# Kernel optimization log

Measured on AMD Instinct MI355X. Metric: run time of the kernel, lower is better.

Reference implementation:

```python
import jax, jax.numpy as jnp
import numpy as np

NUM_EMBEDDINGS = 512
EMBEDDING_DIM = 64
COMMITMENT_COST = 0.25


def setup_inputs() -> dict:
    key = jax.random.key(0)
    k1, k2 = jax.random.split(key)
    inputs = jax.random.normal(k1, (32, EMBEDDING_DIM, 64, 64), dtype=jnp.float32)
    # nn.Embedding weight init: uniform(-1/K, 1/K)
    weight = jax.random.uniform(
        k2, (NUM_EMBEDDINGS, EMBEDDING_DIM), dtype=jnp.float32,
        minval=-1.0 / NUM_EMBEDDINGS, maxval=1.0 / NUM_EMBEDDINGS)
    return {"inputs": inputs, "weight": weight}


def reference(inputs, weight):
    # NCHW -> NHWC
    x = jnp.transpose(inputs, (0, 2, 3, 1))
    B, H, W, D = x.shape
    flat = x.reshape(-1, D)  # [N, D]
    # squared L2 distances to each code: [N, K]
    distances = (jnp.sum(flat * flat, axis=1, keepdims=True)
                 - 2.0 * flat @ weight.T
                 + jnp.sum(weight * weight, axis=1))
    idx = jnp.argmin(distances, axis=1)  # [N]
    # one-hot @ weight == gather (one-hot entries are exactly 0/1)
    quantized = jnp.take(weight, idx, axis=0).reshape(B, H, W, D)
    e_latent_loss = jnp.mean((jax.lax.stop_gradient(quantized) - x) ** 2)
    q_latent_loss = jnp.mean((quantized - jax.lax.stop_gradient(x)) ** 2)
    loss = q_latent_loss + COMMITMENT_COST * e_latent_loss
    # straight-through estimator
    quantized_st = x + jax.lax.stop_gradient(quantized - x)
    discrete_latent = idx.reshape(B, H, W)
    quantized_out = jnp.transpose(quantized_st, (0, 3, 1, 2))  # NHWC -> NCHW
    return discrete_latent, quantized_out, loss
```

## Files before the change

kernel.cpp:

```cpp
#include <hip/hip_runtime.h>

typedef unsigned long long ull;

#define NUM_K   512
#define DIM     64
#define N_ROWS  (32 * 64 * 64)
#define HW      4096
#define CHW     (64 * 4096)

#define IDX_OFF  0
#define Q_OFF    N_ROWS
#define LOSS_OFF (N_ROWS + 32 * 64 * 4096)

#define CAP     8
#define TILE_R  128
#define NBLK    (N_ROWS / TILE_R)

#define WK1S    1.0e-4f
#define WK2S    2.0e-5f

#define WS_W2_OFF    32768
#define WS_W2H_OFF   33280
#define WS_SWMAX_OFF 33792
#define WS_LSL_BYTE  147456
#define WS_NEED      (147456 + NBLK * 8)

typedef __attribute__((ext_vector_type(8)))  short bf16x8;
typedef __attribute__((ext_vector_type(16))) float f32x16;

typedef unsigned uGLB __attribute__((address_space(1)));
typedef unsigned uLDS __attribute__((address_space(3)));
#define GLD16(g, l) __builtin_amdgcn_global_load_lds((const uGLB*)(g), (uLDS*)(l), 16, 0, 0)

#define NP_SUMSQ64(SRC, DST)                                                   \
    do {                                                                       \
        float r_[8];                                                           \
        _Pragma("unroll")                                                      \
        for (int j_ = 0; j_ < 8; ++j_) r_[j_] = __fmul_rn((SRC)[j_], (SRC)[j_]); \
        _Pragma("unroll")                                                      \
        for (int i_ = 8; i_ < 64; i_ += 8) {                                   \
            _Pragma("unroll")                                                  \
            for (int j_ = 0; j_ < 8; ++j_)                                     \
                r_[j_] = __fadd_rn(r_[j_], __fmul_rn((SRC)[i_ + j_], (SRC)[i_ + j_])); \
        }                                                                      \
        (DST) = __fadd_rn(__fadd_rn(__fadd_rn(r_[0], r_[1]), __fadd_rn(r_[2], r_[3])), \
                          __fadd_rn(__fadd_rn(r_[4], r_[5]), __fadd_rn(r_[6], r_[7]))); \
    } while (0)

#define NP_SUMSQ64_G(XC, DST)                                                  \
    do {                                                                       \
        float r_[8];                                                           \
        _Pragma("unroll")                                                      \
        for (int j_ = 0; j_ < 8; ++j_) {                                       \
            float v_ = (XC)[(size_t)j_ * HW];                                  \
            r_[j_] = __fmul_rn(v_, v_);                                        \
        }                                                                      \
        _Pragma("unroll")                                                      \
        for (int i_ = 8; i_ < 64; i_ += 8) {                                   \
            _Pragma("unroll")                                                  \
            for (int j_ = 0; j_ < 8; ++j_) {                                   \
                float v_ = (XC)[(size_t)(i_ + j_) * HW];                       \
                r_[j_] = __fadd_rn(r_[j_], __fmul_rn(v_, v_));                 \
            }                                                                  \
        }                                                                      \
        (DST) = __fadd_rn(__fadd_rn(__fadd_rn(r_[0], r_[1]), __fadd_rn(r_[2], r_[3])), \
                          __fadd_rn(__fadd_rn(r_[4], r_[5]), __fadd_rn(r_[6], r_[7]))); \
    } while (0)

__device__ __forceinline__ unsigned bf16rn(float f) {
    unsigned u = __float_as_uint(f);
    return (u + 0x7fffu + ((u >> 16) & 1u)) >> 16;
}
__device__ __forceinline__ float bf2f(unsigned h) { return __uint_as_float(h << 16); }
__device__ __forceinline__ unsigned pk2(float lo, float hi) {
    return bf16rn(lo) | (bf16rn(hi) << 16);
}

__device__ __forceinline__ float evald(const float* __restrict__ xr,
                                       const float* __restrict__ wc,
                                       float A, float w2c) {
    float m = 0.0f;
    #pragma unroll
    for (int d = 0; d < DIM; ++d) m = __fmaf_rn(xr[d], wc[d], m);
    return __fadd_rn(__fsub_rn(A, __fmul_rn(2.0f, m)), w2c);
}
__device__ __forceinline__ float evald_g(const float* __restrict__ xcol,
                                         const float* __restrict__ wc,
                                         float A, float w2c) {
    float m = 0.0f;
    #pragma unroll
    for (int d = 0; d < DIM; ++d) m = __fmaf_rn(xcol[(size_t)d * HW], wc[d], m);
    return __fadd_rn(__fsub_rn(A, __fmul_rn(2.0f, m)), w2c);
}

__global__ __launch_bounds__(64) void vq_prep8(const float* __restrict__ weight,
                                               unsigned* __restrict__ ws) {
    const int c = blockIdx.x * 64 + threadIdx.x;
    const int T = c >> 5, m = c & 31;
    const float* wr = weight + c * DIM;
    float wv[DIM];
    #pragma unroll
    for (int d = 0; d < DIM; d += 4) {
        float4 t4 = *(const float4*)&wr[d];
        wv[d] = t4.x; wv[d + 1] = t4.y; wv[d + 2] = t4.z; wv[d + 3] = t4.w;
    }
    float s; NP_SUMSQ64(wv, s);
    ((float*)(ws + WS_W2_OFF))[c]  = s;
    ((float*)(ws + WS_W2H_OFF))[c] = 0.5f * s;
    float sa = 0.0f;
    #pragma unroll
    for (int d = 0; d < DIM; ++d) sa = __fadd_rn(sa, fabsf(wv[d]));
    float sv = sa * 1.0002f + 1e-7f;

    #pragma unroll
    for (int s4 = 0; s4 < 4; ++s4) {
        const int gH = (T * 4 + s4) * 2, gL = gH + 1;
        #pragma unroll
        for (int kh = 0; kh < 2; ++kh) {
            unsigned hu[4], lu[4];
            #pragma unroll
            for (int p = 0; p < 4; ++p) {
                float e0 = wv[16 * s4 + 8 * kh + 2 * p];
                float e1 = wv[16 * s4 + 8 * kh + 2 * p + 1];
                unsigned h0 = bf16rn(e0), h1 = bf16rn(e1);
                float r0 = __fsub_rn(e0, bf2f(h0));
                float r1 = __fsub_rn(e1, bf2f(h1));
                hu[p] = h0 | (h1 << 16);
                lu[p] = bf16rn(r0) | (bf16rn(r1) << 16);
            }
            const int slot = (m + 32 * kh) * 4;
            *(uint4*)&ws[gH * 256 + slot] = make_uint4(hu[0], hu[1], hu[2], hu[3]);
            *(uint4*)&ws[gL * 256 + slot] = make_uint4(lu[0], lu[1], lu[2], lu[3]);
        }
    }
    #pragma unroll
    for (int mk = 1; mk <= 32; mk <<= 1) sv = fmaxf(sv, __shfl_xor(sv, mk));
    if (threadIdx.x == 0) ((float*)(ws + WS_SWMAX_OFF))[blockIdx.x] = sv;
}

__global__ __launch_bounds__(256, 3) void vq_mfma8(const float* __restrict__ x_in,
                                                   const float* __restrict__ weight,
                                                   const unsigned* __restrict__ frg,
                                                   const float* __restrict__ w2g,
                                                   const float* __restrict__ w2h,
                                                   double* __restrict__ lslots,
                                                   float* __restrict__ out) {
    __shared__ __align__(16) unsigned dbuf[2][4096];
    __shared__ int   cntL[TILE_R];
    __shared__ unsigned short listL[TILE_R * CAP];
    __shared__ int   ilds[TILE_R];
    __shared__ float wsum[4];

    const int tid   = threadIdx.x;
    const int lane  = tid & 63;
    const int wid   = tid >> 6;
    const int wbase = wid * 32;
    const int n31   = lane & 31;
    const int kh    = lane >> 5;

    const int rowbase = blockIdx.x * TILE_R;
    const int b       = rowbase >> 12;
    const int hw0     = rowbase & 4095;
    const float* xb   = x_in + (size_t)b * CHW + hw0;

    #pragma unroll
    for (int i = 0; i < 4; ++i) {
        int sg = wid * 4 + i;
        GLD16(frg + sg * 256 + lane * 4, &dbuf[0][sg * 256]);
    }

    bf16x8 bh[4], bl[4];
    float mx = 0.0f;
    const float* xp = xb + wbase + n31;
    #pragma unroll
    for (int s = 0; s < 4; ++s) {
        union { unsigned u[4]; bf16x8 v; } ch, cl;
        #pragma unroll
        for (int p = 0; p < 4; ++p) {
            const int k0 = 16 * s + 8 * kh + 2 * p;
            float x0 = xp[(size_t)k0 * HW];
            float x1 = xp[(size_t)(k0 + 1) * HW];
            mx = fmaxf(mx, fmaxf(fabsf(x0), fabsf(x1)));
            float e0 = -x0, e1 = -x1;
            unsigned h0 = bf16rn(e0), h1 = bf16rn(e1);
            float r0 = __fsub_rn(e0, bf2f(h0));
            float r1 = __fsub_rn(e1, bf2f(h1));
            ch.u[p] = h0 | (h1 << 16);
            cl.u[p] = bf16rn(r0) | (bf16rn(r1) << 16);
        }
        bh[s] = ch.v;
        bl[s] = cl.v;
    }
    mx = fmaxf(mx, __shfl_xor(mx, 32));
    if (tid < TILE_R) cntL[tid] = 0;

    const float* swp = (const float*)(frg + WS_SWMAX_OFF);
    float SWMAX = swp[0];
    #pragma unroll
    for (int i = 1; i < 8; ++i) SWMAX = fmaxf(SWMAX, swp[i]);
    const float gthr = __fmaf_rn(WK1S * mx, 2.0f * SWMAX, WK2S);
    float thr = 3.4e38f;
    __syncthreads();

    for (int c = 0; c < 8; ++c) {
        const int par = c & 1;
        if (c < 7) {
            const int nxt = par ^ 1;
            #pragma unroll
            for (int i = 0; i < 4; ++i) {
                int sg = wid * 4 + i;
                GLD16(frg + (c + 1) * 4096 + sg * 256 + lane * 4,
                      &dbuf[nxt][sg * 256]);
            }
        }

        f32x16 acc0, acc1;
        {
            const float* wa = w2h + (2 * c) * 32 + 4 * kh;
            float4 a0 = *(const float4*)&wa[0];
            float4 a1 = *(const float4*)&wa[8];
            float4 a2 = *(const float4*)&wa[16];
            float4 a3 = *(const float4*)&wa[24];
            acc0[0]=a0.x; acc0[1]=a0.y; acc0[2]=a0.z; acc0[3]=a0.w;
            acc0[4]=a1.x; acc0[5]=a1.y; acc0[6]=a1.z; acc0[7]=a1.w;
            acc0[8]=a2.x; acc0[9]=a2.y; acc0[10]=a2.z; acc0[11]=a2.w;
            acc0[12]=a3.x; acc0[13]=a3.y; acc0[14]=a3.z; acc0[15]=a3.w;
            const float* wb = w2h + (2 * c + 1) * 32 + 4 * kh;
            float4 c0 = *(const float4*)&wb[0];
            float4 c1 = *(const float4*)&wb[8];
            float4 c2 = *(const float4*)&wb[16];
            float4 c3 = *(const float4*)&wb[24];
            acc1[0]=c0.x; acc1[1]=c0.y; acc1[2]=c0.z; acc1[3]=c0.w;
            acc1[4]=c1.x; acc1[5]=c1.y; acc1[6]=c1.z; acc1[7]=c1.w;
            acc1[8]=c2.x; acc1[9]=c2.y; acc1[10]=c2.z; acc1[11]=c2.w;
            acc1[12]=c3.x; acc1[13]=c3.y; acc1[14]=c3.z; acc1[15]=c3.w;
        }

        #pragma unroll
        for (int s = 0; s < 4; ++s) {
            bf16x8 ah0 = *(const bf16x8*)&dbuf[par][(s * 2 + 0) * 256 + lane * 4];
            bf16x8 al0 = *(const bf16x8*)&dbuf[par][(s * 2 + 1) * 256 + lane * 4];
            bf16x8 ah1 = *(const bf16x8*)&dbuf[par][(8 * 256) + (s * 2 + 0) * 256 + lane * 4];
            bf16x8 al1 = *(const bf16x8*)&dbuf[par][(8 * 256) + (s * 2 + 1) * 256 + lane * 4];
            acc0 = __builtin_amdgcn_mfma_f32_32x32x16_bf16(ah0, bh[s], acc0, 0, 0, 0);
            acc1 = __builtin_amdgcn_mfma_f32_32x32x16_bf16(ah1, bh[s], acc1, 0, 0, 0);
            acc0 = __builtin_amdgcn_mfma_f32_32x32x16_bf16(al0, bh[s], acc0, 0, 0, 0);
            acc1 = __builtin_amdgcn_mfma_f32_32x32x16_bf16(al1, bh[s], acc1, 0, 0, 0);
            acc0 = __builtin_amdgcn_mfma_f32_32x32x16_bf16(ah0, bl[s], acc0, 0, 0, 0);
            acc1 = __builtin_amdgcn_mfma_f32_32x32x16_bf16(ah1, bl[s], acc1, 0, 0, 0);
        }

        #pragma unroll
        for (int tl = 0; tl < 2; ++tl) {
            float tmin = 3.4e38f;
            #pragma unroll
            for (int r = 0; r < 16; ++r)
                tmin = fminf(tmin, (tl ? acc1[r] : acc0[r]));
            float tlr = fminf(tmin, __shfl_xor(tmin, 32));
            thr = fminf(thr, __fadd_rn(tlr, gthr));
            if (tmin <= thr) {
                const int cb = (2 * c + tl) * 32 + 4 * kh;
                const int rr = wbase + n31;
                #pragma unroll
                for (int r = 0; r < 16; ++r) {
                    float tv = (tl ? acc1[r] : acc0[r]);
                    if (tv <= thr) {
                        int code = cb + (r & 3) + 8 * (r >> 2);
                        int cn = atomicAdd(&cntL[rr], 1);
                        if (cn < CAP) listL[rr * CAP + cn] = (unsigned short)code;
                    }
                }
            }
        }

        __syncthreads();
    }

    if (lane < 32) {
        const int r   = wbase + lane;
        const int cnt = cntL[r];
        if (cnt == 1) {
            int bi = listL[r * CAP];
            ilds[r] = bi;
            out[IDX_OFF + rowbase + r] = (float)bi;
        } else if (cnt >= 2 && cnt <= CAP) {
            const float* xcol = xb + r;
            float A; NP_SUMSQ64_G(xcol, A);
            float bd = 3.4e38f; int bi = 1 << 30;
            for (int t2 = 0; t2 < cnt; ++t2) {
                int cd = listL[r * CAP + t2];
                float d2 = evald_g(xcol, weight + cd * DIM, A, w2g[cd]);
                if (d2 < bd || (d2 == bd && cd < bi)) { bd = d2; bi = cd; }
            }
            ilds[r] = bi;
            out[IDX_OFF + rowbase + r] = (float)bi;
        }
    }
    for (int rr = 0; rr < 32; ++rr) {
        int r   = wbase + rr;
        int cnt = cntL[r];
        if (cnt < 1 || cnt > CAP) {
            const float* xcol = xb + r;
            float A; NP_SUMSQ64_G(xcol, A);
            float bd = 3.4e38f; int bi = 1 << 30;
            #pragma unroll
            for (int t2 = 0; t2 < 8; ++t2) {
                int cd = t2 * 64 + lane;
                float d2 = evald_g(xcol, weight + cd * DIM, A, w2g[cd]);
                if (d2 < bd || (d2 == bd && cd < bi)) { bd = d2; bi = cd; }
            }
            ull key = ((ull)__float_as_uint(bd) << 32) | (unsigned)bi;
            #pragma unroll
            for (int mk = 1; mk <= 32; mk <<= 1) {
                ull o = __shfl_xor(key, mk);
                if (o < key) key = o;
            }
            if (lane == 0) {
                int bi2 = (int)(key & 0xffffffffu);
                ilds[r] = bi2;
                out[IDX_OFF + rowbase + r] = (float)bi2;
            }
        }
    }
    __syncthreads();

    const int row = wbase + (lane & 31);
    const int dh  = (lane >> 5) << 5;
    const float* xcol = xb + row;
    const float* wr2  = weight + ilds[row] * DIM + dh;
    float* ob = out + Q_OFF + (size_t)b * CHW + hw0 + row;
    float lsum = 0.0f;
    #pragma unroll
    for (int j = 0; j < 32; ++j) {
        float xd   = xcol[(size_t)(dh + j) * HW];
        float wq   = wr2[j];
        float diff = __fsub_rn(wq, xd);
        ob[(size_t)(dh + j) * HW] = __fadd_rn(xd, diff);
        lsum = fmaf(diff, diff, lsum);
    }
    #pragma unroll
    for (int off = 32; off > 0; off >>= 1) lsum += __shfl_down(lsum, off);
    if (lane == 0) wsum[wid] = lsum;
    __syncthreads();
    if (tid == 0) {
        double s = 0.0;
        #pragma unroll
        for (int i = 0; i < 4; ++i) s += (double)wsum[i];
        lslots[blockIdx.x] = s;
    }
}

__global__ void vq_finalizeN(const double* __restrict__ lslots, int n,
                             float* __restrict__ out) {
    double s = 0.0;
    for (int i = threadIdx.x; i < n; i += 64) s += lslots[i];
    #pragma unroll
    for (int off = 32; off > 0; off >>= 1) s += __shfl_down(s, off);
    if (threadIdx.x == 0) {
        double m = s / 8388608.0;
        out[LOSS_OFF] = (float)(m + 0.25 * m);
    }
}

__global__ void vq_zero(double* __restrict__ loss_acc) {
    if (threadIdx.x == 0) *loss_acc = 0.0;
}

__global__ __launch_bounds__(256) void vq_fused(const float* __restrict__ x_in,
                                                const float* __restrict__ weight,
                                                double* __restrict__ loss_acc,
                                                float* __restrict__ out) {
    __shared__ float w2s[NUM_K];
    for (int k = threadIdx.x; k < NUM_K; k += 256) {
        const float* wk = weight + k * DIM;
        float s; NP_SUMSQ64(wk, s);
        w2s[k] = s;
    }
    __syncthreads();

    const int n  = blockIdx.x * 256 + threadIdx.x;
    const int b  = n >> 12;
    const int hw = n & 4095;
    const float* xp = x_in + b * CHW + hw;
    float x[DIM];
    #pragma unroll
    for (int d = 0; d < DIM; ++d) x[d] = xp[d * HW];

    float A; NP_SUMSQ64(x, A);

    float best = 3.4e38f;
    int   bi   = 0;
    for (int k = 0; k < NUM_K; k += 4) {
        const float* w0 = weight + k * DIM;
        float m0 = 0.f, m1 = 0.f, m2 = 0.f, m3 = 0.f;
        #pragma unroll
        for (int d = 0; d < DIM; ++d) {
            float xd = x[d];
            m0 = __fmaf_rn(xd, w0[d],           m0);
            m1 = __fmaf_rn(xd, w0[DIM + d],     m1);
            m2 = __fmaf_rn(xd, w0[2 * DIM + d], m2);
            m3 = __fmaf_rn(xd, w0[3 * DIM + d], m3);
        }
        float d0 = __fadd_rn(__fsub_rn(A, __fmul_rn(2.0f, m0)), w2s[k]);
        float d1 = __fadd_rn(__fsub_rn(A, __fmul_rn(2.0f, m1)), w2s[k + 1]);
        float d2 = __fadd_rn(__fsub_rn(A, __fmul_rn(2.0f, m2)), w2s[k + 2]);
        float d3 = __fadd_rn(__fsub_rn(A, __fmul_rn(2.0f, m3)), w2s[k + 3]);
        if (d0 < best) { best = d0; bi = k; }
        if (d1 < best) { best = d1; bi = k + 1; }
        if (d2 < best) { best = d2; bi = k + 2; }
        if (d3 < best) { best = d3; bi = k + 3; }
    }
    const int idx = bi;

    out[IDX_OFF + n] = (float)idx;
    const float* qrow = weight + idx * DIM;
    float* oq = out + Q_OFF + b * CHW + hw;
    float lsum = 0.0f;
    #pragma unroll
    for (int d = 0; d < DIM; ++d) {
        float xd   = xp[d * HW];
        float diff = __fsub_rn(qrow[d], xd);
        oq[d * HW] = __fadd_rn(xd, diff);
        lsum = fmaf(diff, diff, lsum);
    }
    #pragma unroll
    for (int off = 32; off > 0; off >>= 1) lsum += __shfl_down(lsum, off);
    __shared__ float wsum[4];
    if ((threadIdx.x & 63) == 0) wsum[threadIdx.x >> 6] = lsum;
    __syncthreads();
    if (threadIdx.x == 0)
        atomicAdd(loss_acc, (double)((wsum[0] + wsum[1]) + (wsum[2] + wsum[3])));
}

__global__ void vq_finalize(const double* __restrict__ loss_acc,
                            float* __restrict__ out) {
    double m = *loss_acc / 8388608.0;
    out[LOSS_OFF] = (float)(m + 0.25 * m);
}

extern "C" void kernel_launch(void* const* d_in, const int* in_sizes, int n_in,
                              void* d_out, int out_size, void* d_ws, size_t ws_size,
                              hipStream_t stream) {
    const float* x = (const float*)d_in[0];
    const float* w = (const float*)d_in[1];
    float* out = (float*)d_out;

    if (ws_size >= WS_NEED) {
        unsigned* ws32 = (unsigned*)d_ws;
        const float* w2g = (const float*)(ws32 + WS_W2_OFF);
        const float* w2h = (const float*)(ws32 + WS_W2H_OFF);
        double* lslots = (double*)((char*)d_ws + WS_LSL_BYTE);
        vq_prep8<<<8, 64, 0, stream>>>(w, ws32);
        vq_mfma8<<<NBLK, 256, 0, stream>>>(x, w, ws32, w2g, w2h, lslots, out);
        vq_finalizeN<<<1, 64, 0, stream>>>(lslots, NBLK, out);
    } else {
        double* loss_acc = (double*)d_ws;
        vq_zero<<<1, 64, 0, stream>>>(loss_acc);
        vq_fused<<<512, 256, 0, stream>>>(x, w, loss_acc, out);
        vq_finalize<<<1, 1, 0, stream>>>(loss_acc, out);
    }
}
```

Baseline: 158.5 us.

## Build codebook split-bf16 table in LDS per block, drop prep kernel

```diff
diff --git a/kernel.cpp b/kernel.cpp
--- a/kernel.cpp
+++ b/kernel.cpp
@@ -13,24 +13,14 @@
 #define LOSS_OFF (N_ROWS + 32 * 64 * 4096)
 
 #define CAP     8
-#define TILE_R  128
-#define NBLK    (N_ROWS / TILE_R)
+#define TILE_R9 256
+#define NBLK9   (N_ROWS / TILE_R9)
 
 #define WK1S    1.0e-4f
 #define WK2S    2.0e-5f
 
-#define WS_W2_OFF    32768
-#define WS_W2H_OFF   33280
-#define WS_SWMAX_OFF 33792
-#define WS_LSL_BYTE  147456
-#define WS_NEED      (147456 + NBLK * 8)
-
 typedef __attribute__((ext_vector_type(8)))  short bf16x8;
 typedef __attribute__((ext_vector_type(16))) float f32x16;
-
-typedef unsigned uGLB __attribute__((address_space(1)));
-typedef unsigned uLDS __attribute__((address_space(3)));
-#define GLD16(g, l) __builtin_amdgcn_global_load_lds((const uGLB*)(g), (uLDS*)(l), 16, 0, 0)
 
 #define NP_SUMSQ64(SRC, DST)                                                   \
     do {                                                                       \
@@ -72,9 +62,6 @@
     return (u + 0x7fffu + ((u >> 16) & 1u)) >> 16;
 }
 __device__ __forceinline__ float bf2f(unsigned h) { return __uint_as_float(h << 16); }
-__device__ __forceinline__ unsigned pk2(float lo, float hi) {
-    return bf16rn(lo) | (bf16rn(hi) << 16);
-}
 
 __device__ __forceinline__ float evald(const float* __restrict__ xr,
                                        const float* __restrict__ wc,
@@ -93,63 +80,18 @@
     return __fadd_rn(__fsub_rn(A, __fmul_rn(2.0f, m)), w2c);
 }
 
-__global__ __launch_bounds__(64) void vq_prep8(const float* __restrict__ weight,
-                                               unsigned* __restrict__ ws) {
-    const int c = blockIdx.x * 64 + threadIdx.x;
-    const int T = c >> 5, m = c & 31;
-    const float* wr = weight + c * DIM;
-    float wv[DIM];
-    #pragma unroll
-    for (int d = 0; d < DIM; d += 4) {
-        float4 t4 = *(const float4*)&wr[d];
-        wv[d] = t4.x; wv[d + 1] = t4.y; wv[d + 2] = t4.z; wv[d + 3] = t4.w;
-    }
-    float s; NP_SUMSQ64(wv, s);
-    ((float*)(ws + WS_W2_OFF))[c]  = s;
-    ((float*)(ws + WS_W2H_OFF))[c] = 0.5f * s;
-    float sa = 0.0f;
-    #pragma unroll
-    for (int d = 0; d < DIM; ++d) sa = __fadd_rn(sa, fabsf(wv[d]));
-    float sv = sa * 1.0002f + 1e-7f;
-
-    #pragma unroll
-    for (int s4 = 0; s4 < 4; ++s4) {
-        const int gH = (T * 4 + s4) * 2, gL = gH + 1;
-        #pragma unroll
-        for (int kh = 0; kh < 2; ++kh) {
-            unsigned hu[4], lu[4];
-            #pragma unroll
-            for (int p = 0; p < 4; ++p) {
-                float e0 = wv[16 * s4 + 8 * kh + 2 * p];
-                float e1 = wv[16 * s4 + 8 * kh + 2 * p + 1];
-                unsigned h0 = bf16rn(e0), h1 = bf16rn(e1);
-                float r0 = __fsub_rn(e0, bf2f(h0));
-                float r1 = __fsub_rn(e1, bf2f(h1));
-                hu[p] = h0 | (h1 << 16);
-                lu[p] = bf16rn(r0) | (bf16rn(r1) << 16);
-            }
-            const int slot = (m + 32 * kh) * 4;
-            *(uint4*)&ws[gH * 256 + slot] = make_uint4(hu[0], hu[1], hu[2], hu[3]);
-            *(uint4*)&ws[gL * 256 + slot] = make_uint4(lu[0], lu[1], lu[2], lu[3]);
-        }
-    }
-    #pragma unroll
-    for (int mk = 1; mk <= 32; mk <<= 1) sv = fmaxf(sv, __shfl_xor(sv, mk));
-    if (threadIdx.x == 0) ((float*)(ws + WS_SWMAX_OFF))[blockIdx.x] = sv;
-}
-
-__global__ __launch_bounds__(256, 3) void vq_mfma8(const float* __restrict__ x_in,
+__global__ __launch_bounds__(512, 1) void vq_mfma9(const float* __restrict__ x_in,
                                                    const float* __restrict__ weight,
-                                                   const unsigned* __restrict__ frg,
-                                                   const float* __restrict__ w2g,
-                                                   const float* __restrict__ w2h,
                                                    double* __restrict__ lslots,
                                                    float* __restrict__ out) {
-    __shared__ __align__(16) unsigned dbuf[2][4096];
-    __shared__ int   cntL[TILE_R];
-    __shared__ unsigned short listL[TILE_R * CAP];
-    __shared__ int   ilds[TILE_R];
-    __shared__ float wsum[4];
+    __shared__ __align__(16) unsigned tbl[32768];
+    __shared__ float w2h_l[NUM_K];
+    __shared__ float w2a_l[NUM_K];
+    __shared__ float swred[8];
+    __shared__ int   cntL[TILE_R9];
+    __shared__ unsigned short listL[TILE_R9 * CAP];
+    __shared__ int   ilds[TILE_R9];
+    __shared__ float wsum[8];
 
     const int tid   = threadIdx.x;
     const int lane  = tid & 63;
@@ -158,16 +100,60 @@
     const int n31   = lane & 31;
     const int kh    = lane >> 5;
 
-    const int rowbase = blockIdx.x * TILE_R;
+    const int rowbase = blockIdx.x * TILE_R9;
     const int b       = rowbase >> 12;
     const int hw0     = rowbase & 4095;
     const float* xb   = x_in + (size_t)b * CHW + hw0;
 
-    #pragma unroll
-    for (int i = 0; i < 4; ++i) {
-        int sg = wid * 4 + i;
-        GLD16(frg + sg * 256 + lane * 4, &dbuf[0][sg * 256]);
-    }
+    {
+        const int c = tid;
+        const int T = c >> 5, m = c & 31;
+        const float* wr = weight + c * DIM;
+        float wv[DIM];
+        #pragma unroll
+        for (int d = 0; d < DIM; d += 4) {
+            float4 t4 = *(const float4*)&wr[d];
+            wv[d] = t4.x; wv[d + 1] = t4.y; wv[d + 2] = t4.z; wv[d + 3] = t4.w;
+        }
+        float s; NP_SUMSQ64(wv, s);
+        w2a_l[c] = s;
+        w2h_l[c] = 0.5f * s;
+        float sa = 0.0f;
+        #pragma unroll
+        for (int d = 0; d < DIM; ++d) sa = __fadd_rn(sa, fabsf(wv[d]));
+        float sv = sa * 1.0002f + 1e-7f;
+
+        #pragma unroll
+        for (int s4 = 0; s4 < 4; ++s4) {
+            const int gH = T * 8 + s4 * 2, gL = gH + 1;
+            #pragma unroll
+            for (int k2 = 0; k2 < 2; ++k2) {
+                unsigned hu[4], lu[4];
+                #pragma unroll
+                for (int p = 0; p < 4; ++p) {
+                    float e0 = wv[16 * s4 + 8 * k2 + 2 * p];
+                    float e1 = wv[16 * s4 + 8 * k2 + 2 * p + 1];
+                    unsigned h0 = bf16rn(e0), h1 = bf16rn(e1);
+                    float r0 = __fsub_rn(e0, bf2f(h0));
+                    float r1 = __fsub_rn(e1, bf2f(h1));
+                    hu[p] = h0 | (h1 << 16);
+                    lu[p] = bf16rn(r0) | (bf16rn(r1) << 16);
+                }
+                const int slot = (m + 32 * k2) * 4;
+                *(uint4*)&tbl[gH * 256 + slot] = make_uint4(hu[0], hu[1], hu[2], hu[3]);
+                *(uint4*)&tbl[gL * 256 + slot] = make_uint4(lu[0], lu[1], lu[2], lu[3]);
+            }
+        }
+        #pragma unroll
+        for (int mk = 1; mk <= 32; mk <<= 1) sv = fmaxf(sv, __shfl_xor(sv, mk));
+        if (lane == 0) swred[wid] = sv;
+        if (tid < TILE_R9) cntL[tid] = 0;
+    }
+    __syncthreads();
+
+    float SWMAX = swred[0];
+    #pragma unroll
+    for (int i = 1; i < 8; ++i) SWMAX = fmaxf(SWMAX, swred[i]);
 
     bf16x8 bh[4], bl[4];
     float mx = 0.0f;
@@ -192,31 +178,13 @@
         bl[s] = cl.v;
     }
     mx = fmaxf(mx, __shfl_xor(mx, 32));
-    if (tid < TILE_R) cntL[tid] = 0;
-
-    const float* swp = (const float*)(frg + WS_SWMAX_OFF);
-    float SWMAX = swp[0];
-    #pragma unroll
-    for (int i = 1; i < 8; ++i) SWMAX = fmaxf(SWMAX, swp[i]);
     const float gthr = __fmaf_rn(WK1S * mx, 2.0f * SWMAX, WK2S);
     float thr = 3.4e38f;
-    __syncthreads();
 
     for (int c = 0; c < 8; ++c) {
-        const int par = c & 1;
-        if (c < 7) {
-            const int nxt = par ^ 1;
-            #pragma unroll
-            for (int i = 0; i < 4; ++i) {
-                int sg = wid * 4 + i;
-                GLD16(frg + (c + 1) * 4096 + sg * 256 + lane * 4,
-                      &dbuf[nxt][sg * 256]);
-            }
-        }
-
         f32x16 acc0, acc1;
         {
-            const float* wa = w2h + (2 * c) * 32 + 4 * kh;
+            const float* wa = &w2h_l[(2 * c) * 32 + 4 * kh];
             float4 a0 = *(const float4*)&wa[0];
             float4 a1 = *(const float4*)&wa[8];
             float4 a2 = *(const float4*)&wa[16];
@@ -225,7 +193,7 @@
             acc0[4]=a1.x; acc0[5]=a1.y; acc0[6]=a1.z; acc0[7]=a1.w;
             acc0[8]=a2.x; acc0[9]=a2.y; acc0[10]=a2.z; acc0[11]=a2.w;
             acc0[12]=a3.x; acc0[13]=a3.y; acc0[14]=a3.z; acc0[15]=a3.w;
-            const float* wb = w2h + (2 * c + 1) * 32 + 4 * kh;
+            const float* wb = &w2h_l[(2 * c + 1) * 32 + 4 * kh];
             float4 c0 = *(const float4*)&wb[0];
             float4 c1 = *(const float4*)&wb[8];
             float4 c2 = *(const float4*)&wb[16];
@@ -236,12 +204,13 @@
             acc1[12]=c3.x; acc1[13]=c3.y; acc1[14]=c3.z; acc1[15]=c3.w;
         }
 
+        const unsigned* base = &tbl[c * 16 * 256];
         #pragma unroll
         for (int s = 0; s < 4; ++s) {
-            bf16x8 ah0 = *(const bf16x8*)&dbuf[par][(s * 2 + 0) * 256 + lane * 4];
-            bf16x8 al0 = *(const bf16x8*)&dbuf[par][(s * 2 + 1) * 256 + lane * 4];
-            bf16x8 ah1 = *(const bf16x8*)&dbuf[par][(8 * 256) + (s * 2 + 0) * 256 + lane * 4];
-            bf16x8 al1 = *(const bf16x8*)&dbuf[par][(8 * 256) + (s * 2 + 1) * 256 + lane * 4];
+            bf16x8 ah0 = *(const bf16x8*)&base[(s * 2 + 0) * 256 + lane * 4];
+            bf16x8 al0 = *(const bf16x8*)&base[(s * 2 + 1) * 256 + lane * 4];
+            bf16x8 ah1 = *(const bf16x8*)&base[(8 + s * 2 + 0) * 256 + lane * 4];
+            bf16x8 al1 = *(const bf16x8*)&base[(8 + s * 2 + 1) * 256 + lane * 4];
             acc0 = __builtin_amdgcn_mfma_f32_32x32x16_bf16(ah0, bh[s], acc0, 0, 0, 0);
             acc1 = __builtin_amdgcn_mfma_f32_32x32x16_bf16(ah1, bh[s], acc1, 0, 0, 0);
             acc0 = __builtin_amdgcn_mfma_f32_32x32x16_bf16(al0, bh[s], acc0, 0, 0, 0);
@@ -272,9 +241,9 @@
                 }
             }
         }
-
-        __syncthreads();
-    }
+    }
+
+    __syncthreads();
 
     if (lane < 32) {
         const int r   = wbase + lane;
@@ -289,7 +258,7 @@
             float bd = 3.4e38f; int bi = 1 << 30;
             for (int t2 = 0; t2 < cnt; ++t2) {
                 int cd = listL[r * CAP + t2];
-                float d2 = evald_g(xcol, weight + cd * DIM, A, w2g[cd]);
+                float d2 = evald_g(xcol, weight + cd * DIM, A, w2a_l[cd]);
                 if (d2 < bd || (d2 == bd && cd < bi)) { bd = d2; bi = cd; }
             }
             ilds[r] = bi;
@@ -306,7 +275,7 @@
             #pragma unroll
             for (int t2 = 0; t2 < 8; ++t2) {
                 int cd = t2 * 64 + lane;
-                float d2 = evald_g(xcol, weight + cd * DIM, A, w2g[cd]);
+                float d2 = evald_g(xcol, weight + cd * DIM, A, w2a_l[cd]);
                 if (d2 < bd || (d2 == bd && cd < bi)) { bd = d2; bi = cd; }
             }
             ull key = ((ull)__float_as_uint(bd) << 32) | (unsigned)bi;
@@ -345,7 +314,7 @@
     if (tid == 0) {
         double s = 0.0;
         #pragma unroll
-        for (int i = 0; i < 4; ++i) s += (double)wsum[i];
+        for (int i = 0; i < 8; ++i) s += (double)wsum[i];
         lslots[blockIdx.x] = s;
     }
 }
@@ -445,14 +414,10 @@
     const float* w = (const float*)d_in[1];
     float* out = (float*)d_out;
 
-    if (ws_size >= WS_NEED) {
-        unsigned* ws32 = (unsigned*)d_ws;
-        const float* w2g = (const float*)(ws32 + WS_W2_OFF);
-        const float* w2h = (const float*)(ws32 + WS_W2H_OFF);
-        double* lslots = (double*)((char*)d_ws + WS_LSL_BYTE);
-        vq_prep8<<<8, 64, 0, stream>>>(w, ws32);
-        vq_mfma8<<<NBLK, 256, 0, stream>>>(x, w, ws32, w2g, w2h, lslots, out);
-        vq_finalizeN<<<1, 64, 0, stream>>>(lslots, NBLK, out);
+    if (ws_size >= NBLK9 * sizeof(double)) {
+        double* lslots = (double*)d_ws;
+        vq_mfma9<<<NBLK9, 512, 0, stream>>>(x, w, lslots, out);
+        vq_finalizeN<<<1, 64, 0, stream>>>(lslots, NBLK9, out);
     } else {
         double* loss_acc = (double*)d_ws;
         vq_zero<<<1, 64, 0, stream>>>(loss_acc);
```

Result: slower. 172.6 us (+8.9%).
